# Kernel optimization log

Hardware: AMD Instinct MI355X
Metric: run time of the kernel (lower is better)

The kernel has to match this reference:

```python
import jax, jax.numpy as jnp
import numpy as np

N_EMBD = 768
N_HEAD = 12

def setup_inputs() -> dict:
    key = jax.random.key(0)
    k_x, k_wa, k_ba, k_wp, k_bp = jax.random.split(key, 5)
    C = N_EMBD
    scale = 1.0 / np.sqrt(C)
    return {
        "x": jax.random.normal(k_x, (2, 4096, C), dtype=jnp.float32),
        "W_attn": jax.random.normal(k_wa, (C, 3 * C), dtype=jnp.float32) * scale,
        "b_attn": jax.random.normal(k_ba, (3 * C,), dtype=jnp.float32) * 0.01,
        "W_proj": jax.random.normal(k_wp, (C, C), dtype=jnp.float32) * scale,
        "b_proj": jax.random.normal(k_bp, (C,), dtype=jnp.float32) * 0.01,
    }

def reference(x, W_attn, b_attn, W_proj, b_proj) -> jnp.ndarray:
    B, T, C = x.shape
    H = N_HEAD
    D = C // H  # head dim
    qkv = x @ W_attn + b_attn                     # [B,T,3C]
    q, k, v = jnp.split(qkv, 3, axis=-1)
    # [B,T,C] -> [B,H,T,D]
    q = q.reshape(B, T, H, D).transpose(0, 2, 1, 3)
    k = k.reshape(B, T, H, D).transpose(0, 2, 1, 3)
    v = v.reshape(B, T, H, D).transpose(0, 2, 1, 3)
    scores = jnp.einsum("bhqd,bhkd->bhqk", q, k) * (1.0 / jnp.sqrt(jnp.float32(D)))
    attn = jax.nn.softmax(scores, axis=-1)        # dropout p=0.0 -> identity
    y = jnp.einsum("bhqk,bhkd->bhqd", attn, v)    # [B,H,T,D]
    y = y.transpose(0, 2, 1, 3).reshape(B, T, C)
    return y @ W_proj + b_proj
```

## Files before the change

kernel.cpp:

```cpp
#include <hip/hip_runtime.h>
#include <stdint.h>

#define NB 2
#define NT 4096
#define NC 768
#define NH 12
#define ND 64
#define NBT (NB*NT)
#define NQKV (3*NC)

typedef _Float16 half_t;
typedef __attribute__((ext_vector_type(8))) _Float16 f16x8;
typedef __attribute__((ext_vector_type(4))) _Float16 f16x4;
typedef __attribute__((ext_vector_type(2))) __fp16 fp16x2;
typedef __attribute__((ext_vector_type(4))) float f32x4;

#define MFMA16(a,b,c) __builtin_amdgcn_mfma_f32_16x16x32_f16((a),(b),(c),0,0,0)

__device__ __forceinline__ void load_lds16(const void* g, void* l) {
    auto gp = reinterpret_cast<__attribute__((address_space(1))) char*>(reinterpret_cast<uintptr_t>(g));
    auto lp = reinterpret_cast<__attribute__((address_space(3))) char*>(reinterpret_cast<uintptr_t>(l));
    __builtin_amdgcn_global_load_lds(gp, lp, 16, 0, 0);
}

__global__ __launch_bounds__(256) void k_pack(const float* __restrict__ in, half_t* __restrict__ out, int n4) {
    int i = blockIdx.x * 256 + threadIdx.x;
    if (i >= n4) return;
    float4 f = reinterpret_cast<const float4*>(in)[i];
    f16x4 h;
    h[0] = (half_t)f.x; h[1] = (half_t)f.y; h[2] = (half_t)f.z; h[3] = (half_t)f.w;
    reinterpret_cast<f16x4*>(out)[i] = h;
}

__global__ __launch_bounds__(256) void k_packT(const float* __restrict__ in, half_t* __restrict__ out, int N, int K) {
    int idx = blockIdx.x * 256 + threadIdx.x;
    if (idx >= N * K) return;
    int n = idx / K, k = idx - n * K;
    out[idx] = (half_t)in[(size_t)k * N + n];
}

template<int OUTF32>
__global__ __launch_bounds__(256) void k_gemm(const half_t* __restrict__ A, const half_t* __restrict__ Bt,
                                              const float* __restrict__ bias, void* __restrict__ out, int N) {
    __shared__ half_t As[128 * 32];
    __shared__ half_t Bs[128 * 32];
    const int tid = threadIdx.x;
    const int lane = tid & 63, w = tid >> 6;
    const int m0 = blockIdx.x * 128, n0 = blockIdx.y * 128;
    const int wm = (w >> 1) * 64, wn = (w & 1) * 64;
    const int lr = lane & 15, lk = (lane >> 4) * 8;

    f32x4 acc[4][4];
#pragma unroll
    for (int a = 0; a < 4; ++a)
#pragma unroll
        for (int bq = 0; bq < 4; ++bq) acc[a][bq] = (f32x4){0.f, 0.f, 0.f, 0.f};

    const int c0 = tid, c1 = 256 + tid;
    const int ldsbase = (tid & ~63) * 16;

    for (int ks = 0; ks < 24; ++ks) {
        const int k0 = ks * 32;
        __syncthreads();
        load_lds16(A  + (size_t)(m0 + (c0 >> 2)) * NC + k0 + (c0 & 3) * 8, (char*)As + ldsbase);
        load_lds16(Bt + (size_t)(n0 + (c0 >> 2)) * NC + k0 + (c0 & 3) * 8, (char*)Bs + ldsbase);
        load_lds16(A  + (size_t)(m0 + (c1 >> 2)) * NC + k0 + (c1 & 3) * 8, (char*)As + 4096 + ldsbase);
        load_lds16(Bt + (size_t)(n0 + (c1 >> 2)) * NC + k0 + (c1 & 3) * 8, (char*)Bs + 4096 + ldsbase);
        __syncthreads();
        f16x8 af[4], bf[4];
#pragma unroll
        for (int mi = 0; mi < 4; ++mi)
            af[mi] = *reinterpret_cast<const f16x8*>(&As[(wm + mi * 16 + lr) * 32 + lk]);
#pragma unroll
        for (int ni = 0; ni < 4; ++ni)
            bf[ni] = *reinterpret_cast<const f16x8*>(&Bs[(wn + ni * 16 + lr) * 32 + lk]);
#pragma unroll
        for (int mi = 0; mi < 4; ++mi)
#pragma unroll
            for (int ni = 0; ni < 4; ++ni)
                acc[mi][ni] = MFMA16(af[mi], bf[ni], acc[mi][ni]);
    }

    const int rg = (lane >> 4) * 4;
#pragma unroll
    for (int ni = 0; ni < 4; ++ni) {
        const int gn = n0 + wn + ni * 16 + lr;
        const float bv = bias[gn];
#pragma unroll
        for (int mi = 0; mi < 4; ++mi)
#pragma unroll
            for (int i = 0; i < 4; ++i) {
                const size_t gm = (size_t)(m0 + wm + mi * 16 + rg + i);
                const float v = acc[mi][ni][i] + bv;
                if (OUTF32) reinterpret_cast<float*>(out)[gm * N + gn] = v;
                else        reinterpret_cast<half_t*>(out)[gm * N + gn] = (half_t)v;
            }
    }
}

__global__ __launch_bounds__(256) void k_vt(const half_t* __restrict__ qkv, half_t* __restrict__ Vt) {
    __shared__ half_t tile[64][72];
    const int tid = threadIdx.x;
    const int t0 = blockIdx.x * 64, bh = blockIdx.y;
    const int b = bh / NH, h = bh - b * NH;
    {
        const int tl = tid >> 2, dc = (tid & 3) * 16;
        const half_t* src = qkv + (size_t)(b * NT + t0 + tl) * NQKV + 2 * NC + h * ND + dc;
        f16x8 v0 = *reinterpret_cast<const f16x8*>(src);
        f16x8 v1 = *reinterpret_cast<const f16x8*>(src + 8);
        *reinterpret_cast<f16x8*>(&tile[tl][dc]) = v0;
        *reinterpret_cast<f16x8*>(&tile[tl][dc + 8]) = v1;
    }
    __syncthreads();
    {
        const int d = tid >> 2, tc = (tid & 3) * 16;
        half_t* dst = Vt + ((size_t)bh * ND + d) * NT + t0 + tc;
        f16x8 o0, o1;
#pragma unroll
        for (int j = 0; j < 8; ++j) o0[j] = tile[tc + j][d];
#pragma unroll
        for (int j = 0; j < 8; ++j) o1[j] = tile[tc + 8 + j][d];
        *reinterpret_cast<f16x8*>(dst) = o0;
        *reinterpret_cast<f16x8*>(dst + 8) = o1;
    }
}

struct __align__(16) AttnSmem {
    union {
        struct { half_t K[2][64 * 64]; half_t V[2][64 * 64]; } m;
        struct { float y[2][64][64]; float l[2][64][4]; } r;
    };
};

__global__ __launch_bounds__(256, 3) void k_attn(const half_t* __restrict__ qkv, const half_t* __restrict__ Vt,
                                                 half_t* __restrict__ Y) {
    __shared__ AttnSmem sm;
    const int tid = threadIdx.x, lane = tid & 63, w = tid >> 6;
    const int qw = w & 1, kw = w >> 1;
    const int lr = lane & 15, g = lane >> 4;
    const int qt = blockIdx.x, bh = blockIdx.y;
    const int b = bh / NH, h = bh - b * NH;
    const half_t* Qp = qkv + (size_t)b * NT * NQKV + h * ND;
    const half_t* Kp = Qp + NC;
    const half_t* Vbase = Vt + (size_t)bh * ND * NT;
    const int q0 = qt * 128 + qw * 64;

    const int sr = tid >> 3;
    const int colh = (((tid & 7) << 3)) ^ ((sr & 7) << 3);
    const int wub = (tid & ~63) * 16;

    f16x8 aq[4][2];
    const half_t cch = (half_t)(0.125f * 1.4426950408889634f);
#pragma unroll
    for (int qf = 0; qf < 4; ++qf)
#pragma unroll
        for (int dh = 0; dh < 2; ++dh) {
            aq[qf][dh] = *reinterpret_cast<const f16x8*>(&Qp[(size_t)(q0 + qf * 16 + lr) * NQKV + dh * 32 + g * 8]);
#pragma unroll
            for (int j = 0; j < 8; ++j) aq[qf][dh][j] = aq[qf][dh][j] * cch;
        }

    const int swk = (lr & 7) << 3;
    const int cA = (g * 8) ^ swk;
    const int cB = (32 + g * 8) ^ swk;
    const int psw = lr & 7;
    const int goff = (g & 1) << 2;
    const int vcol[2] = { (((g >> 1) + 4 * kw + 0) ^ psw) * 8 + goff,
                          (((g >> 1) + 4 * kw + 2) ^ psw) * 8 + goff };

    f32x4 y[4][4];
#pragma unroll
    for (int qf = 0; qf < 4; ++qf)
#pragma unroll
        for (int df = 0; df < 4; ++df) y[qf][df] = (f32x4){0.f, 0.f, 0.f, 0.f};
    float l_[4] = {0.f, 0.f, 0.f, 0.f};

    auto stagebuf = [&](int buf, const half_t* Ks, const half_t* Vs) {
        char* kdst = (char*)&sm.m.K[buf][0] + wub;
        char* vdst = (char*)&sm.m.V[buf][0] + wub;
        load_lds16(Ks, kdst);
        load_lds16(Ks + (size_t)32 * NQKV, kdst + 4096);
        load_lds16(Vs, vdst);
        load_lds16(Vs + (size_t)32 * NT, vdst + 4096);
    };

    const half_t* ksrc = Kp + (size_t)sr * NQKV + colh;
    const half_t* vsrc = Vbase + (size_t)sr * NT + colh;
    stagebuf(0, ksrc, vsrc);
    ksrc += (size_t)64 * NQKV;
    vsrc += 64;
    __syncthreads();
    int cur = 0;
    const int stb = 2 * kw;

    for (int t = 0; t < NT / 64; ++t) {
        if (t < NT / 64 - 1) {
            stagebuf(cur ^ 1, ksrc, vsrc);
            ksrc += (size_t)64 * NQKV;
            vsrc += 64;
        }

        f32x4 s[4][2];
#pragma unroll
        for (int qf = 0; qf < 4; ++qf) { s[qf][0] = (f32x4){0.f,0.f,0.f,0.f}; s[qf][1] = (f32x4){0.f,0.f,0.f,0.f}; }
        const half_t* Kc = &sm.m.K[cur][0];
        __builtin_amdgcn_s_setprio(1);
#pragma unroll
        for (int sl = 0; sl < 2; ++sl) {
            const int row = (stb + sl) * 16 + lr;
            f16x8 bk0 = *reinterpret_cast<const f16x8*>(&Kc[row * 64 + cA]);
            s[0][sl] = MFMA16(bk0, aq[0][0], s[0][sl]);
            s[1][sl] = MFMA16(bk0, aq[1][0], s[1][sl]);
            s[2][sl] = MFMA16(bk0, aq[2][0], s[2][sl]);
            s[3][sl] = MFMA16(bk0, aq[3][0], s[3][sl]);
            f16x8 bk1 = *reinterpret_cast<const f16x8*>(&Kc[row * 64 + cB]);
            s[0][sl] = MFMA16(bk1, aq[0][1], s[0][sl]);
            s[1][sl] = MFMA16(bk1, aq[1][1], s[1][sl]);
            s[2][sl] = MFMA16(bk1, aq[2][1], s[2][sl]);
            s[3][sl] = MFMA16(bk1, aq[3][1], s[3][sl]);
        }
        __builtin_amdgcn_s_setprio(0);

        f16x8 pb[4];
#pragma unroll
        for (int qf = 0; qf < 4; ++qf) {
            float ps = 0.f;
            union { f16x8 v; fp16x2 h[4]; } u;
#pragma unroll
            for (int hs = 0; hs < 2; ++hs) {
                const float p0 = __builtin_amdgcn_exp2f(s[qf][hs][0]);
                const float p1 = __builtin_amdgcn_exp2f(s[qf][hs][1]);
                const float p2 = __builtin_amdgcn_exp2f(s[qf][hs][2]);
                const float p3 = __builtin_amdgcn_exp2f(s[qf][hs][3]);
                u.h[2 * hs]     = __builtin_amdgcn_cvt_pkrtz(p0, p1);
                u.h[2 * hs + 1] = __builtin_amdgcn_cvt_pkrtz(p2, p3);
                ps += (p0 + p1) + (p2 + p3);
            }
            pb[qf] = u.v;
            l_[qf] += ps;
        }

        const half_t* Vc = &sm.m.V[cur][0];
        __builtin_amdgcn_s_setprio(1);
#pragma unroll
        for (int df = 0; df < 4; ++df) {
            const half_t* vrow = &Vc[(df * 16 + lr) * 64];
            union { f16x8 v; f16x4 q[2]; } va;
            va.q[0] = *reinterpret_cast<const f16x4*>(vrow + vcol[0]);
            va.q[1] = *reinterpret_cast<const f16x4*>(vrow + vcol[1]);
            y[0][df] = MFMA16(va.v, pb[0], y[0][df]);
            y[1][df] = MFMA16(va.v, pb[1], y[1][df]);
            y[2][df] = MFMA16(va.v, pb[2], y[2][df]);
            y[3][df] = MFMA16(va.v, pb[3], y[3][df]);
        }
        __builtin_amdgcn_s_setprio(0);

        __syncthreads();
        cur ^= 1;
    }

    if (kw == 1) {
#pragma unroll
        for (int qf = 0; qf < 4; ++qf)
#pragma unroll
            for (int df = 0; df < 4; ++df) {
                const int jb = (qf * 16 + df * 4) ^ ((lane & 7) << 2);
                *reinterpret_cast<f32x4*>(&sm.r.y[qw][lane][jb]) = y[qf][df];
            }
#pragma unroll
        for (int qf = 0; qf < 4; ++qf) sm.r.l[qw][lane][qf] = l_[qf];
    }
    __syncthreads();
    if (kw == 0) {
#pragma unroll
        for (int qf = 0; qf < 4; ++qf) {
#pragma unroll
            for (int df = 0; df < 4; ++df) {
                const int jb = (qf * 16 + df * 4) ^ ((lane & 7) << 2);
                const f32x4 yp = *reinterpret_cast<const f32x4*>(&sm.r.y[qw][lane][jb]);
                y[qf][df] += yp;
            }
            float l = l_[qf] + sm.r.l[qw][lane][qf];
            l += __shfl_xor(l, 16);
            l += __shfl_xor(l, 32);
            const float rl = 1.f / l;
            half_t* Yp = Y + (size_t)(b * NT + q0 + qf * 16 + lr) * NC + h * ND + g * 4;
#pragma unroll
            for (int df = 0; df < 4; ++df) {
                union { f16x4 v; fp16x2 hh[2]; } o;
                o.hh[0] = __builtin_amdgcn_cvt_pkrtz(y[qf][df][0] * rl, y[qf][df][1] * rl);
                o.hh[1] = __builtin_amdgcn_cvt_pkrtz(y[qf][df][2] * rl, y[qf][df][3] * rl);
                *reinterpret_cast<f16x4*>(Yp + df * 16) = o.v;
            }
        }
    }
}

extern "C" void kernel_launch(void* const* d_in, const int* in_sizes, int n_in,
                              void* d_out, int out_size, void* d_ws, size_t ws_size,
                              hipStream_t stream) {
    const float* x  = (const float*)d_in[0];
    const float* Wa = (const float*)d_in[1];
    const float* ba = (const float*)d_in[2];
    const float* Wp = (const float*)d_in[3];
    const float* bp = (const float*)d_in[4];
    float* out = (float*)d_out;

    char* ws = (char*)d_ws;
    half_t* xh   = (half_t*)ws; ws += (size_t)NBT * NC * 2;
    half_t* Wat  = (half_t*)ws; ws += (size_t)NQKV * NC * 2;
    half_t* Wpt  = (half_t*)ws; ws += (size_t)NC * NC * 2;
    half_t* qkvh = (half_t*)ws; ws += (size_t)NBT * NQKV * 2;
    half_t* vt   = (half_t*)ws; ws += (size_t)NB * NH * ND * NT * 2;
    half_t* yh   = (half_t*)ws; ws += (size_t)NBT * NC * 2;

    k_pack<<<(NBT * NC / 4 + 255) / 256, 256, 0, stream>>>(x, xh, NBT * NC / 4);
    k_packT<<<(NQKV * NC + 255) / 256, 256, 0, stream>>>(Wa, Wat, NQKV, NC);
    k_packT<<<(NC * NC + 255) / 256, 256, 0, stream>>>(Wp, Wpt, NC, NC);
    k_gemm<0><<<dim3(NBT / 128, NQKV / 128), 256, 0, stream>>>(xh, Wat, ba, qkvh, NQKV);
    k_vt<<<dim3(NT / 64, NB * NH), 256, 0, stream>>>(qkvh, vt);
    k_attn<<<dim3(NT / 128, NB * NH), 256, 0, stream>>>(qkvh, vt, yh);
    k_gemm<1><<<dim3(NBT / 128, NC / 128), 256, 0, stream>>>(yh, Wpt, bp, out, NC);
}
```

Baseline: 206.0 us.

## Double-buffer GEMM LDS tiles and interleave softmax exp with PV MFMAs

The QKV/projection GEMM now uses two LDS buffers, prefetching the next K-slice with global_load_lds while the MFMAs run on the current slice, and needs one barrier per iteration instead of two. In the attention kernel, the V fragments are loaded up front and each query fragment's PV MFMAs are issued right after its exp2/pack, so exp and MFMA work can overlap. The cost is twice the LDS in the GEMM, which may lower occupancy, plus more live registers for the V fragments in attention.

```diff
diff --git a/kernel.cpp b/kernel.cpp
--- a/kernel.cpp
+++ b/kernel.cpp
@@ -42,8 +42,8 @@
 template<int OUTF32>
 __global__ __launch_bounds__(256) void k_gemm(const half_t* __restrict__ A, const half_t* __restrict__ Bt,
                                               const float* __restrict__ bias, void* __restrict__ out, int N) {
-    __shared__ half_t As[128 * 32];
-    __shared__ half_t Bs[128 * 32];
+    __shared__ half_t As[2][128 * 32];
+    __shared__ half_t Bs[2][128 * 32];
     const int tid = threadIdx.x;
     const int lane = tid & 63, w = tid >> 6;
     const int m0 = blockIdx.x * 128, n0 = blockIdx.y * 128;
@@ -58,27 +58,38 @@
 
     const int c0 = tid, c1 = 256 + tid;
     const int ldsbase = (tid & ~63) * 16;
+    const half_t* A0 = A  + (size_t)(m0 + (c0 >> 2)) * NC + (c0 & 3) * 8;
+    const half_t* A1 = A  + (size_t)(m0 + (c1 >> 2)) * NC + (c1 & 3) * 8;
+    const half_t* B0 = Bt + (size_t)(n0 + (c0 >> 2)) * NC + (c0 & 3) * 8;
+    const half_t* B1 = Bt + (size_t)(n0 + (c1 >> 2)) * NC + (c1 & 3) * 8;
+
+    auto stage = [&](int buf, int k0) {
+        load_lds16(A0 + k0, (char*)&As[buf][0] + ldsbase);
+        load_lds16(B0 + k0, (char*)&Bs[buf][0] + ldsbase);
+        load_lds16(A1 + k0, (char*)&As[buf][0] + 4096 + ldsbase);
+        load_lds16(B1 + k0, (char*)&Bs[buf][0] + 4096 + ldsbase);
+    };
+
+    stage(0, 0);
+    __syncthreads();
+    int cur = 0;
 
     for (int ks = 0; ks < 24; ++ks) {
-        const int k0 = ks * 32;
-        __syncthreads();
-        load_lds16(A  + (size_t)(m0 + (c0 >> 2)) * NC + k0 + (c0 & 3) * 8, (char*)As + ldsbase);
-        load_lds16(Bt + (size_t)(n0 + (c0 >> 2)) * NC + k0 + (c0 & 3) * 8, (char*)Bs + ldsbase);
-        load_lds16(A  + (size_t)(m0 + (c1 >> 2)) * NC + k0 + (c1 & 3) * 8, (char*)As + 4096 + ldsbase);
-        load_lds16(Bt + (size_t)(n0 + (c1 >> 2)) * NC + k0 + (c1 & 3) * 8, (char*)Bs + 4096 + ldsbase);
-        __syncthreads();
+        if (ks < 23) stage(cur ^ 1, (ks + 1) * 32);
         f16x8 af[4], bf[4];
 #pragma unroll
         for (int mi = 0; mi < 4; ++mi)
-            af[mi] = *reinterpret_cast<const f16x8*>(&As[(wm + mi * 16 + lr) * 32 + lk]);
+            af[mi] = *reinterpret_cast<const f16x8*>(&As[cur][(wm + mi * 16 + lr) * 32 + lk]);
 #pragma unroll
         for (int ni = 0; ni < 4; ++ni)
-            bf[ni] = *reinterpret_cast<const f16x8*>(&Bs[(wn + ni * 16 + lr) * 32 + lk]);
+            bf[ni] = *reinterpret_cast<const f16x8*>(&Bs[cur][(wn + ni * 16 + lr) * 32 + lk]);
 #pragma unroll
         for (int mi = 0; mi < 4; ++mi)
 #pragma unroll
             for (int ni = 0; ni < 4; ++ni)
                 acc[mi][ni] = MFMA16(af[mi], bf[ni], acc[mi][ni]);
+        __syncthreads();
+        cur ^= 1;
     }
 
     const int rg = (lane >> 4) * 4;
@@ -221,7 +232,15 @@
         }
         __builtin_amdgcn_s_setprio(0);
 
-        f16x8 pb[4];
+        const half_t* Vc = &sm.m.V[cur][0];
+        union { f16x8 v; f16x4 q[2]; } va[4];
+#pragma unroll
+        for (int df = 0; df < 4; ++df) {
+            const half_t* vrow = &Vc[(df * 16 + lr) * 64];
+            va[df].q[0] = *reinterpret_cast<const f16x4*>(vrow + vcol[0]);
+            va[df].q[1] = *reinterpret_cast<const f16x4*>(vrow + vcol[1]);
+        }
+
 #pragma unroll
         for (int qf = 0; qf < 4; ++qf) {
             float ps = 0.f;
@@ -236,24 +255,14 @@
                 u.h[2 * hs + 1] = __builtin_amdgcn_cvt_pkrtz(p2, p3);
                 ps += (p0 + p1) + (p2 + p3);
             }
-            pb[qf] = u.v;
             l_[qf] += ps;
-        }
-
-        const half_t* Vc = &sm.m.V[cur][0];
-        __builtin_amdgcn_s_setprio(1);
-#pragma unroll
-        for (int df = 0; df < 4; ++df) {
-            const half_t* vrow = &Vc[(df * 16 + lr) * 64];
-            union { f16x8 v; f16x4 q[2]; } va;
-            va.q[0] = *reinterpret_cast<const f16x4*>(vrow + vcol[0]);
-            va.q[1] = *reinterpret_cast<const f16x4*>(vrow + vcol[1]);
-            y[0][df] = MFMA16(va.v, pb[0], y[0][df]);
-            y[1][df] = MFMA16(va.v, pb[1], y[1][df]);
-            y[2][df] = MFMA16(va.v, pb[2], y[2][df]);
-            y[3][df] = MFMA16(va.v, pb[3], y[3][df]);
-        }
-        __builtin_amdgcn_s_setprio(0);
+            __builtin_amdgcn_s_setprio(1);
+            y[qf][0] = MFMA16(va[0].v, u.v, y[qf][0]);
+            y[qf][1] = MFMA16(va[1].v, u.v, y[qf][1]);
+            y[qf][2] = MFMA16(va[2].v, u.v, y[qf][2]);
+            y[qf][3] = MFMA16(va[3].v, u.v, y[qf][3]);
+            __builtin_amdgcn_s_setprio(0);
+        }
 
         __syncthreads();
         cur ^= 1;
```

Result: slower. 226.1 us (+9.8%).
